# Optimization experiments

Hardware: AMD Instinct MI355X
Metric: run time of the kernel (lower is better)

The kernel has to match this reference:

```python
import jax, jax.numpy as jnp
import numpy as np

HIDDEN = 32          # hardcoded in nn.Linear(latent_dim, 32)
THRESHOLD = 1.5      # hardcoded adjacency threshold


def setup_inputs() -> dict:
    key = jax.random.key(0)
    ks = jax.random.split(key, 12)
    N, LATENT, MSG = 8192, 128, 64

    def lin(kw, kb, fan_in, fan_out):
        bound = 1.0 / np.sqrt(fan_in)
        W = jax.random.uniform(kw, (fan_in, fan_out), jnp.float32, -bound, bound)
        b = jax.random.uniform(kb, (fan_out,), jnp.float32, -bound, bound)
        return W, b

    enc_W, enc_b = lin(ks[0], ks[1], LATENT, HIDDEN)
    msg_W, msg_b = lin(ks[2], ks[3], HIDDEN, MSG)
    upd_W, upd_b = lin(ks[4], ks[5], HIDDEN + MSG, HIDDEN)
    out_W, out_b = lin(ks[6], ks[7], HIDDEN, MSG)

    z = jax.random.normal(ks[8], (N, LATENT), jnp.float32)
    agent_dists = jax.random.normal(ks[9], (N, N), jnp.float32)
    tau = jnp.float32(1.0)
    return {
        "z": z, "tau": tau, "agent_dists": agent_dists,
        "enc_W": enc_W, "enc_b": enc_b,
        "msg_W": msg_W, "msg_b": msg_b,
        "upd_W": upd_W, "upd_b": upd_b,
        "out_W": out_W, "out_b": out_b,
    }


def reference(z, tau, agent_dists, enc_W, enc_b, msg_W, msg_b, upd_W, upd_b, out_W, out_b):
    N = agent_dists.shape[0]
    h = jax.nn.relu(z @ enc_W + enc_b)                       # [N, 32]
    # vectorized adjacency: off-diagonal entries with dist < threshold
    idx = jnp.arange(N)
    off_diag = idx[:, None] != idx[None, :]
    adj = jnp.where(off_diag & (agent_dists < THRESHOLD), 1.0, 0.0).astype(z.dtype)  # [N, N]
    messages = h @ msg_W + msg_b                             # [N, MSG]
    aggregated = adj @ messages                              # [N, MSG]
    h2 = jax.nn.relu(jnp.concatenate([h, aggregated], axis=-1) @ upd_W + upd_b)  # [N, 32]
    logits = h2 @ out_W + out_b                              # [N, MSG]
    # gumbel_softmax (soft): softmax((logits + gumbel) / tau)
    gkey = jax.random.key(42)
    u = jax.random.uniform(gkey, logits.shape, logits.dtype, 1e-10, 1.0)
    gumbel = -jnp.log(-jnp.log(u))
    return jax.nn.softmax((logits + gumbel) / tau, axis=-1)
```

## Files before the change

### kernel.cpp

```cpp
#include <hip/hip_runtime.h>
#include <hip/hip_bf16.h>
#include <math.h>

#define N_AGENTS 8192
#define LATENT   128
#define HIDDEN   32
#define MSG      64
#define CONCAT   96
#define THRESH   1.5f
#define KSPLIT   16

typedef float f32x4  __attribute__((ext_vector_type(4)));
typedef short bf16x8 __attribute__((ext_vector_type(8)));

__device__ __forceinline__ unsigned rotl32(unsigned x, unsigned r) {
  return (x << r) | (x >> (32u - r));
}
__device__ __forceinline__ void tf_round(unsigned &x0, unsigned &x1, unsigned r) {
  x0 += x1; x1 = rotl32(x1, r); x1 ^= x0;
}
__device__ __forceinline__ uint2 threefry_0_42(unsigned x0, unsigned x1) {
  const unsigned k0 = 0u, k1 = 42u, k2 = 0x1BD11BDAu ^ 0u ^ 42u;
  x0 += k0; x1 += k1;
  tf_round(x0,x1,13); tf_round(x0,x1,15); tf_round(x0,x1,26); tf_round(x0,x1, 6);
  x0 += k1; x1 += k2 + 1u;
  tf_round(x0,x1,17); tf_round(x0,x1,29); tf_round(x0,x1,16); tf_round(x0,x1,24);
  x0 += k2; x1 += k0 + 2u;
  tf_round(x0,x1,13); tf_round(x0,x1,15); tf_round(x0,x1,26); tf_round(x0,x1, 6);
  x0 += k0; x1 += k1 + 3u;
  tf_round(x0,x1,17); tf_round(x0,x1,29); tf_round(x0,x1,16); tf_round(x0,x1,24);
  x0 += k1; x1 += k2 + 4u;
  tf_round(x0,x1,13); tf_round(x0,x1,15); tf_round(x0,x1,26); tf_round(x0,x1, 6);
  x0 += k2; x1 += k0 + 5u;
  return make_uint2(x0, x1);
}

__device__ __forceinline__ float gumbel_at(unsigned idx) {
  const unsigned H = (N_AGENTS * MSG) / 2;
  unsigned bits;
  if (idx < H) {
    uint2 o = threefry_0_42(idx, idx + H);
    bits = o.x;
  } else {
    uint2 o = threefry_0_42(idx - H, idx);
    bits = o.y;
  }
  float f = __uint_as_float((bits >> 9) | 0x3f800000u) - 1.0f;
  float u = fmaxf(1e-10f, f + 1e-10f);
  return -logf(-logf(u));
}

__device__ __forceinline__ unsigned short f2bf(float x) {
  unsigned u = __float_as_uint(x);
  u += 0x7FFFu + ((u >> 16) & 1u);
  return (unsigned short)(u >> 16);
}

__global__ __launch_bounds__(256) void k_encode(
    const float* __restrict__ z, const float* __restrict__ encW, const float* __restrict__ encB,
    const float* __restrict__ msgW, const float* __restrict__ msgB,
    float* __restrict__ h_out, unsigned* __restrict__ msgR_u32,
    unsigned short* __restrict__ msgT)
{
  __shared__ float z_s[8][LATENT];
  __shared__ float encW_s[LATENT*HIDDEN];
  __shared__ float msgW_s[HIDDEN*MSG];
  __shared__ float h_s[8][HIDDEN];
  __shared__ float m_s[8][MSG];
  const int t  = threadIdx.x;
  const int r0 = blockIdx.x * 8;

  #pragma unroll
  for (int it = 0; it < 16; ++it) encW_s[t + 256*it] = encW[t + 256*it];
  #pragma unroll
  for (int it = 0; it < 8; ++it)  msgW_s[t + 256*it] = msgW[t + 256*it];
  #pragma unroll
  for (int it = 0; it < 4; ++it) {
    int q = t + 256*it;
    z_s[q >> 7][q & 127] = z[(size_t)r0*LATENT + q];
  }
  __syncthreads();

  {
    int r = t >> 5, c = t & 31;
    float acc = encB[c];
    #pragma unroll
    for (int k = 0; k < LATENT; ++k) acc = fmaf(z_s[r][k], encW_s[k*HIDDEN + c], acc);
    float hv = fmaxf(acc, 0.0f);
    h_s[r][c] = hv;
    h_out[(size_t)(r0 + r)*HIDDEN + c] = hv;
  }
  __syncthreads();

  #pragma unroll
  for (int it = 0; it < 2; ++it) {
    int r = (t >> 6) + 4*it, c = t & 63;
    float acc = msgB[c];
    #pragma unroll
    for (int k = 0; k < HIDDEN; ++k) acc = fmaf(h_s[r][k], msgW_s[k*MSG + c], acc);
    m_s[r][c] = acc;
  }
  __syncthreads();

  {
    int r = t >> 5, c0 = (t & 31) * 2;
    unsigned lo = f2bf(m_s[r][c0]), hi = f2bf(m_s[r][c0 + 1]);
    msgR_u32[(size_t)(r0 + r)*32 + (t & 31)] = lo | (hi << 16);
  }
  {
    int c = t & 63, rr = (t >> 6) * 2;
    unsigned lo = f2bf(m_s[rr][c]), hi = f2bf(m_s[rr + 1][c]);
    *(unsigned*)(msgT + (size_t)c*N_AGENTS + r0 + rr) = lo | (hi << 16);
  }
}

__device__ __forceinline__ bf16x8 adj_frag(f32x4 lo, f32x4 hi) {
  union { bf16x8 v; unsigned u[4]; } r;
  r.u[0] = (lo.x < THRESH ? 0x3F80u : 0u) | (lo.y < THRESH ? 0x3F800000u : 0u);
  r.u[1] = (lo.z < THRESH ? 0x3F80u : 0u) | (lo.w < THRESH ? 0x3F800000u : 0u);
  r.u[2] = (hi.x < THRESH ? 0x3F80u : 0u) | (hi.y < THRESH ? 0x3F800000u : 0u);
  r.u[3] = (hi.z < THRESH ? 0x3F80u : 0u) | (hi.w < THRESH ? 0x3F800000u : 0u);
  return r.v;
}

__global__ __launch_bounds__(256, 4) void k_agg(
    const float* __restrict__ dists, const unsigned short* __restrict__ msgT,
    float* __restrict__ C)
{
  const int lane = threadIdx.x & 63;
  const int wv   = threadIdx.x >> 6;
  const int W    = blockIdx.x * 4 + wv;
  const int rowTile = W & 255;
  const int kslice  = W >> 8;
  const int row0 = rowTile * 32;
  const int k0   = kslice * (N_AGENTS / KSPLIT);
  const int m = lane & 15, q = lane >> 4;

  const float* a0p = dists + (size_t)(row0 + m) * N_AGENTS + k0 + q*8;
  const float* a1p = a0p + (size_t)16 * N_AGENTS;
  const unsigned short* b0p = msgT + (size_t)(m)      * N_AGENTS + k0 + q*8;
  const unsigned short* b1p = msgT + (size_t)(m + 16) * N_AGENTS + k0 + q*8;
  const unsigned short* b2p = msgT + (size_t)(m + 32) * N_AGENTS + k0 + q*8;
  const unsigned short* b3p = msgT + (size_t)(m + 48) * N_AGENTS + k0 + q*8;

  f32x4 acc[2][4];
  #pragma unroll
  for (int g = 0; g < 2; ++g)
    #pragma unroll
    for (int nt = 0; nt < 4; ++nt) acc[g][nt] = (f32x4)0.0f;

  #pragma unroll
  for (int kk = 0; kk < (N_AGENTS / KSPLIT) / 32; ++kk) {
    const int off = kk * 32;
    f32x4 a00 = __builtin_nontemporal_load((const f32x4*)(a0p + off));
    f32x4 a01 = __builtin_nontemporal_load((const f32x4*)(a0p + off + 4));
    f32x4 a10 = __builtin_nontemporal_load((const f32x4*)(a1p + off));
    f32x4 a11 = __builtin_nontemporal_load((const f32x4*)(a1p + off + 4));
    bf16x8 b0 = *(const bf16x8*)(b0p + off);
    bf16x8 b1 = *(const bf16x8*)(b1p + off);
    bf16x8 b2 = *(const bf16x8*)(b2p + off);
    bf16x8 b3 = *(const bf16x8*)(b3p + off);
    bf16x8 af0 = adj_frag(a00, a01);
    bf16x8 af1 = adj_frag(a10, a11);
    acc[0][0] = __builtin_amdgcn_mfma_f32_16x16x32_bf16(af0, b0, acc[0][0], 0, 0, 0);
    acc[0][1] = __builtin_amdgcn_mfma_f32_16x16x32_bf16(af0, b1, acc[0][1], 0, 0, 0);
    acc[0][2] = __builtin_amdgcn_mfma_f32_16x16x32_bf16(af0, b2, acc[0][2], 0, 0, 0);
    acc[0][3] = __builtin_amdgcn_mfma_f32_16x16x32_bf16(af0, b3, acc[0][3], 0, 0, 0);
    acc[1][0] = __builtin_amdgcn_mfma_f32_16x16x32_bf16(af1, b0, acc[1][0], 0, 0, 0);
    acc[1][1] = __builtin_amdgcn_mfma_f32_16x16x32_bf16(af1, b1, acc[1][1], 0, 0, 0);
    acc[1][2] = __builtin_amdgcn_mfma_f32_16x16x32_bf16(af1, b2, acc[1][2], 0, 0, 0);
    acc[1][3] = __builtin_amdgcn_mfma_f32_16x16x32_bf16(af1, b3, acc[1][3], 0, 0, 0);
  }

  #pragma unroll
  for (int g = 0; g < 2; ++g)
    #pragma unroll
    for (int nt = 0; nt < 4; ++nt)
      #pragma unroll
      for (int r = 0; r < 4; ++r)
        atomicAdd(&C[(size_t)(row0 + g*16 + q*4 + r) * MSG + nt*16 + m], acc[g][nt][r]);
}

__global__ __launch_bounds__(256) void k_out(
    const float* __restrict__ C, const float* __restrict__ dists,
    const unsigned short* __restrict__ msgR,
    const float* __restrict__ h_in,
    const float* __restrict__ updW, const float* __restrict__ updB,
    const float* __restrict__ outW, const float* __restrict__ outB,
    const float* __restrict__ tau, float* __restrict__ out)
{
  __shared__ float x_s[4][CONCAT];
  __shared__ float h2_s[4][HIDDEN];
  const int w    = threadIdx.x >> 6;
  const int lane = threadIdx.x & 63;
  const int i    = blockIdx.x * 4 + w;

  float agg = C[(size_t)i * MSG + lane];
  float dii = dists[(size_t)i * (N_AGENTS + 1)];
  if (dii < THRESH) {
    unsigned short us = msgR[(size_t)i * MSG + lane];
    agg -= __uint_as_float(((unsigned)us) << 16);
  }

  x_s[w][HIDDEN + lane] = agg;
  if (lane < HIDDEN) x_s[w][lane] = h_in[(size_t)i * HIDDEN + lane];
  __syncthreads();

  if (lane < HIDDEN) {
    float acc = updB[lane];
    #pragma unroll
    for (int k = 0; k < CONCAT; ++k) acc = fmaf(x_s[w][k], updW[k*HIDDEN + lane], acc);
    h2_s[w][lane] = fmaxf(acc, 0.0f);
  }
  __syncthreads();

  float lg = outB[lane];
  #pragma unroll
  for (int c = 0; c < HIDDEN; ++c) lg = fmaf(h2_s[w][c], outW[c*MSG + lane], lg);

  float tv = (lg + gumbel_at((unsigned)i*64u + (unsigned)lane)) / tau[0];

  float mx = tv;
  #pragma unroll
  for (int off = 32; off > 0; off >>= 1) mx = fmaxf(mx, __shfl_xor(mx, off, 64));
  float ex = expf(tv - mx);
  float sm = ex;
  #pragma unroll
  for (int off = 32; off > 0; off >>= 1) sm += __shfl_xor(sm, off, 64);
  out[(size_t)i * MSG + lane] = ex / sm;
}

extern "C" void kernel_launch(void* const* d_in, const int* in_sizes, int n_in,
                              void* d_out, int out_size, void* d_ws, size_t ws_size,
                              hipStream_t stream) {
  const float* z     = (const float*)d_in[0];
  const float* tau   = (const float*)d_in[1];
  const float* dists = (const float*)d_in[2];
  const float* encW  = (const float*)d_in[3];
  const float* encB  = (const float*)d_in[4];
  const float* msgW  = (const float*)d_in[5];
  const float* msgB  = (const float*)d_in[6];
  const float* updW  = (const float*)d_in[7];
  const float* updB  = (const float*)d_in[8];
  const float* outW  = (const float*)d_in[9];
  const float* outB  = (const float*)d_in[10];
  (void)in_sizes; (void)n_in; (void)out_size; (void)ws_size;

  char* ws = (char*)d_ws;
  float*          C_ws  = (float*)(ws);
  float*          h_ws  = (float*)(ws + (2u<<20));
  unsigned short* msgR  = (unsigned short*)(ws + (3u<<20));
  unsigned short* msgT  = (unsigned short*)(ws + (4u<<20));
  float* out = (float*)d_out;

  hipMemsetAsync(C_ws, 0, (size_t)N_AGENTS * MSG * sizeof(float), stream);
  hipLaunchKernelGGL(k_encode, dim3(N_AGENTS/8), dim3(256), 0, stream,
                     z, encW, encB, msgW, msgB, h_ws, (unsigned*)msgR, msgT);
  hipLaunchKernelGGL(k_agg, dim3((256 * KSPLIT) / 4), dim3(256), 0, stream,
                     dists, msgT, C_ws);
  hipLaunchKernelGGL(k_out, dim3(N_AGENTS/4), dim3(256), 0, stream,
                     C_ws, dists, msgR, h_ws, updW, updB, outW, outB, tau, out);
}
```

Before: 428.4 us.

## Replace split-K atomics with in-block LDS reduction and partial buffers

```diff
diff --git a/kernel.cpp b/kernel.cpp
--- a/kernel.cpp
+++ b/kernel.cpp
@@ -9,6 +9,8 @@
 #define CONCAT   96
 #define THRESH   1.5f
 #define KSPLIT   16
+#define SLICE    (N_AGENTS / KSPLIT)
+#define SGRP     4
 
 typedef float f32x4  __attribute__((ext_vector_type(4)));
 typedef short bf16x8 __attribute__((ext_vector_type(8)));
@@ -125,15 +127,15 @@
 
 __global__ __launch_bounds__(256, 4) void k_agg(
     const float* __restrict__ dists, const unsigned short* __restrict__ msgT,
-    float* __restrict__ C)
+    float* __restrict__ P)
 {
+  __shared__ float red_s[4][32][MSG];
   const int lane = threadIdx.x & 63;
   const int wv   = threadIdx.x >> 6;
-  const int W    = blockIdx.x * 4 + wv;
-  const int rowTile = W & 255;
-  const int kslice  = W >> 8;
+  const int rowTile  = blockIdx.x & 255;
+  const int sliceGrp = blockIdx.x >> 8;
   const int row0 = rowTile * 32;
-  const int k0   = kslice * (N_AGENTS / KSPLIT);
+  const int k0   = (sliceGrp * 4 + wv) * SLICE;
   const int m = lane & 15, q = lane >> 4;
 
   const float* a0p = dists + (size_t)(row0 + m) * N_AGENTS + k0 + q*8;
@@ -150,7 +152,7 @@
     for (int nt = 0; nt < 4; ++nt) acc[g][nt] = (f32x4)0.0f;
 
   #pragma unroll
-  for (int kk = 0; kk < (N_AGENTS / KSPLIT) / 32; ++kk) {
+  for (int kk = 0; kk < SLICE / 32; ++kk) {
     const int off = kk * 32;
     f32x4 a00 = __builtin_nontemporal_load((const f32x4*)(a0p + off));
     f32x4 a01 = __builtin_nontemporal_load((const f32x4*)(a0p + off + 4));
@@ -178,11 +180,25 @@
     for (int nt = 0; nt < 4; ++nt)
       #pragma unroll
       for (int r = 0; r < 4; ++r)
-        atomicAdd(&C[(size_t)(row0 + g*16 + q*4 + r) * MSG + nt*16 + m], acc[g][nt][r]);
+        red_s[wv][g*16 + q*4 + r][nt*16 + m] = acc[g][nt][r];
+  __syncthreads();
+
+  const int row = threadIdx.x >> 3;
+  const int c0  = (threadIdx.x & 7) * 8;
+  f32x4 s0 = *(const f32x4*)&red_s[0][row][c0];
+  f32x4 s1 = *(const f32x4*)&red_s[0][row][c0 + 4];
+  #pragma unroll
+  for (int w2 = 1; w2 < 4; ++w2) {
+    s0 += *(const f32x4*)&red_s[w2][row][c0];
+    s1 += *(const f32x4*)&red_s[w2][row][c0 + 4];
+  }
+  float* dst = P + ((size_t)sliceGrp * N_AGENTS + row0 + row) * MSG + c0;
+  *(f32x4*)dst       = s0;
+  *(f32x4*)(dst + 4) = s1;
 }
 
 __global__ __launch_bounds__(256) void k_out(
-    const float* __restrict__ C, const float* __restrict__ dists,
+    const float* __restrict__ P, const float* __restrict__ dists,
     const unsigned short* __restrict__ msgR,
     const float* __restrict__ h_in,
     const float* __restrict__ updW, const float* __restrict__ updB,
@@ -195,7 +211,11 @@
   const int lane = threadIdx.x & 63;
   const int i    = blockIdx.x * 4 + w;
 
-  float agg = C[(size_t)i * MSG + lane];
+  float agg = 0.0f;
+  #pragma unroll
+  for (int g = 0; g < SGRP; ++g)
+    agg += P[((size_t)g * N_AGENTS + i) * MSG + lane];
+
   float dii = dists[(size_t)i * (N_AGENTS + 1)];
   if (dii < THRESH) {
     unsigned short us = msgR[(size_t)i * MSG + lane];
@@ -247,17 +267,16 @@
   (void)in_sizes; (void)n_in; (void)out_size; (void)ws_size;
 
   char* ws = (char*)d_ws;
-  float*          C_ws  = (float*)(ws);
-  float*          h_ws  = (float*)(ws + (2u<<20));
-  unsigned short* msgR  = (unsigned short*)(ws + (3u<<20));
-  unsigned short* msgT  = (unsigned short*)(ws + (4u<<20));
+  float*          P_ws  = (float*)(ws);
+  float*          h_ws  = (float*)(ws + (8u<<20));
+  unsigned short* msgR  = (unsigned short*)(ws + (9u<<20));
+  unsigned short* msgT  = (unsigned short*)(ws + (10u<<20));
   float* out = (float*)d_out;
 
-  hipMemsetAsync(C_ws, 0, (size_t)N_AGENTS * MSG * sizeof(float), stream);
   hipLaunchKernelGGL(k_encode, dim3(N_AGENTS/8), dim3(256), 0, stream,
                      z, encW, encB, msgW, msgB, h_ws, (unsigned*)msgR, msgT);
-  hipLaunchKernelGGL(k_agg, dim3((256 * KSPLIT) / 4), dim3(256), 0, stream,
-                     dists, msgT, C_ws);
+  hipLaunchKernelGGL(k_agg, dim3(256 * SGRP), dim3(256), 0, stream,
+                     dists, msgT, P_ws);
   hipLaunchKernelGGL(k_out, dim3(N_AGENTS/4), dim3(256), 0, stream,
-                     C_ws, dists, msgR, h_ws, updW, updB, outW, outB, tau, out);
-}
+                     P_ws, dists, msgR, h_ws, updW, updB, outW, outB, tau, out);
+}
```

Measured after the change: 430.6 us. No clear change (+0.5%).
